# Optimization experiments

Measured on AMD Instinct MI355X. Metric: run time of the kernel, lower is better.

The kernel has to match this reference:

```python
import jax, jax.numpy as jnp
import numpy as np

N_NODES = 50000
N_EDGES = 800000
D_FEAT = 64
K_HOPS = 8


def setup_inputs() -> dict:
    key = jax.random.key(0)
    k1, k2 = jax.random.split(key)
    feature = jax.random.normal(k1, (N_NODES, D_FEAT), dtype=jnp.float32)
    edge_index = jax.random.randint(k2, (2, N_EDGES), 0, N_NODES, dtype=jnp.int32)
    return {"feature": feature, "edge_index": edge_index}


def reference(feature, edge_index):
    # with A_hat = D^{-1/2} (A + I) D^{-1/2} (add_remaining_self_loops + sym_norm).
    n = feature.shape[0]
    src, dst = edge_index[0], edge_index[1]
    # add_remaining_self_loops: drop any existing self-loop edges (weight -> 0)
    # and append a self loop of weight fill_value=1 for every node. Zeroing the
    # weight is mathematically identical to removing the edge.
    ew = jnp.where(src == dst, 0.0, 1.0).astype(feature.dtype)
    loop = jnp.arange(n, dtype=src.dtype)
    row = jnp.concatenate([src, loop])          # message source (x_j)
    col = jnp.concatenate([dst, loop])          # aggregation target (i)
    w = jnp.concatenate([ew, jnp.ones((n,), dtype=feature.dtype)])
    # symmetric normalization: deg over row, norm = d^-1/2[row] * w * d^-1/2[col]
    deg = jax.ops.segment_sum(w, row, num_segments=n)
    deg_inv_sqrt = jnp.where(deg > 0, jax.lax.rsqrt(deg), 0.0)
    norm = deg_inv_sqrt[row] * w * deg_inv_sqrt[col]  # [E+N]

    xs = [feature]
    x = feature
    for _ in range(K_HOPS):  # small fixed K, structural loop
        # gather-scale-scatter_add: out[i] = sum_{(j,i) in E} norm * x[j]
        x = jax.ops.segment_sum(norm[:, None] * x[row], col, num_segments=n)
        xs.append(x)
    return jnp.concatenate(xs, axis=1)  # [N, (K+1)*D]
```

## Files before the change

kernel.cpp:

```cpp
#include <hip/hip_runtime.h>
#include <hip/hip_fp16.h>

#define N_NODES 50000
#define N_EDGES 800000
#define D_FEAT 64
#define K_HOPS 8
#define OUT_STRIDE ((K_HOPS + 1) * D_FEAT)
#define NPART 128
#define CHUNK (N_EDGES / NPART)
#define NWORD (N_NODES / 2)

#define SCAN_WORDS 512
#define SCAN_NB ((NWORD + SCAN_WORDS - 1) / SCAN_WORDS)

#define ALIGN256(x) (((x) + 255) & ~(size_t)255)
static const size_t OFF_PSRC  = 0;
static const size_t OFF_PDST  = OFF_PSRC  + (size_t)NPART * NWORD * 4;
static const size_t OFF_BASES = OFF_PDST  + (size_t)NPART * NWORD * 4;
static const size_t OFF_OFF   = ALIGN256(OFF_BASES + (size_t)NPART * N_NODES * 4);
static const size_t OFF_BSUM  = ALIGN256(OFF_OFF   + (size_t)(N_NODES + 1) * 4);
static const size_t OFF_TOTW  = ALIGN256(OFF_BSUM  + 64 * 4);
static const size_t OFF_DINV  = ALIGN256(OFF_TOTW  + (size_t)NWORD * 4);
static const size_t OFF_CSR   = ALIGN256(OFF_DINV  + (size_t)N_NODES * 4);
static const size_t OFF_XA    = ALIGN256(OFF_CSR   + (size_t)N_EDGES * 4);
static const size_t OFF_XB    = ALIGN256(OFF_XA + (size_t)(N_NODES + 1) * D_FEAT * 2);

__device__ __forceinline__ unsigned pack_h2(float a, float b) {
    union { __half2 h; unsigned u; } c;
    c.h = __floats2half2_rn(a, b);
    return c.u;
}
__device__ __forceinline__ float2 unpack_h2(unsigned u) {
    union { unsigned u; __half2 h; } c;
    c.u = u;
    return __half22float2(c.h);
}


__global__ __launch_bounds__(256, 1) void k_hist(const int* __restrict__ src,
                                                 const int* __restrict__ dst,
                                                 unsigned* __restrict__ psrc,
                                                 unsigned* __restrict__ pdst) {
    __shared__ unsigned h[NWORD];
    int t = threadIdx.x;
    int base = blockIdx.x * CHUNK;
    for (int w = t; w < NWORD; w += 256) h[w] = 0u;
    __syncthreads();
    for (int j = t; j < CHUNK; j += 256) {
        int s = src[base + j], d = dst[base + j];
        if (s != d) atomicAdd(&h[s >> 1], (s & 1) ? 65536u : 1u);
    }
    __syncthreads();
    unsigned* o1 = psrc + (size_t)blockIdx.x * NWORD;
    for (int w = t; w < NWORD; w += 256) o1[w] = h[w];
    __syncthreads();
    for (int w = t; w < NWORD; w += 256) h[w] = 0u;
    __syncthreads();
    for (int j = t; j < CHUNK; j += 256) {
        int s = src[base + j], d = dst[base + j];
        if (s != d) atomicAdd(&h[d >> 1], (d & 1) ? 65536u : 1u);
    }
    __syncthreads();
    unsigned* o2 = pdst + (size_t)blockIdx.x * NWORD;
    for (int w = t; w < NWORD; w += 256) o2[w] = h[w];
}

__global__ void k_deg(const unsigned* __restrict__ psrc, float* __restrict__ dinv) {
    int w = blockIdx.x * blockDim.x + threadIdx.x;
    if (w >= NWORD) return;
    unsigned s0 = 0, s1 = 0, s2 = 0, s3 = 0;
    #pragma unroll 4
    for (int c = 0; c < NPART; c += 4) {
        s0 += psrc[(size_t)(c + 0) * NWORD + w];
        s1 += psrc[(size_t)(c + 1) * NWORD + w];
        s2 += psrc[(size_t)(c + 2) * NWORD + w];
        s3 += psrc[(size_t)(c + 3) * NWORD + w];
    }
    unsigned s = (s0 + s1) + (s2 + s3);
    dinv[2 * w + 0] = rsqrtf((float)((s & 0xffffu) + 1u));
    dinv[2 * w + 1] = rsqrtf((float)((s >> 16) + 1u));
}

__global__ void k_tot(const unsigned* __restrict__ pdst, unsigned* __restrict__ totW) {
    int w = blockIdx.x * blockDim.x + threadIdx.x;
    if (w >= NWORD) return;
    unsigned s0 = 0, s1 = 0, s2 = 0, s3 = 0;
    #pragma unroll 4
    for (int c = 0; c < NPART; c += 4) {
        s0 += pdst[(size_t)(c + 0) * NWORD + w];
        s1 += pdst[(size_t)(c + 1) * NWORD + w];
        s2 += pdst[(size_t)(c + 2) * NWORD + w];
        s3 += pdst[(size_t)(c + 3) * NWORD + w];
    }
    totW[w] = (s0 + s1) + (s2 + s3);
}

__global__ void k_scan_sums(const unsigned* __restrict__ totW, int* __restrict__ bsum) {
    __shared__ int lds[256];
    int b = blockIdx.x, t = threadIdx.x;
    int wend = min((b + 1) * SCAN_WORDS, NWORD);
    int tot = 0;
    for (int w = b * SCAN_WORDS + t; w < wend; w += 256) {
        unsigned v = totW[w];
        tot += (int)(v & 0xffffu) + (int)(v >> 16);
    }
    lds[t] = tot; __syncthreads();
    for (int str = 128; str > 0; str >>= 1) {
        if (t < str) lds[t] += lds[t + str];
        __syncthreads();
    }
    if (t == 0) bsum[b] = lds[0];
}

__global__ void k_scan_top(int* __restrict__ bsum) {
    int lane = threadIdx.x;
    int orig = (lane < SCAN_NB) ? bsum[lane] : 0;
    int v = orig;
    for (int d = 1; d < 64; d <<= 1) {
        int u = __shfl_up(v, d, 64);
        if (lane >= d) v += u;
    }
    if (lane < SCAN_NB) bsum[lane] = v - orig;
}

__global__ void k_scan_downA(const unsigned* __restrict__ totW, const int* __restrict__ bsum,
                             int* __restrict__ off) {
    __shared__ int lds[256];
    int b = blockIdx.x, t = threadIdx.x;
    int w0 = b * SCAN_WORDS + 2 * t;
    unsigned t0 = (w0 < NWORD) ? totW[w0] : 0u;
    unsigned t1 = (w0 + 1 < NWORD) ? totW[w0 + 1] : 0u;
    int n[4] = { (int)(t0 & 0xffffu), (int)(t0 >> 16),
                 (int)(t1 & 0xffffu), (int)(t1 >> 16) };
    int tsum = (n[0] + n[1]) + (n[2] + n[3]);
    lds[t] = tsum; __syncthreads();
    int x = tsum;
    for (int d = 1; d < 256; d <<= 1) {
        int u = (t >= d) ? lds[t - d] : 0;
        __syncthreads();
        x += u;
        lds[t] = x;
        __syncthreads();
    }
    int p = (x - tsum) + bsum[b];
    #pragma unroll
    for (int j = 0; j < 4; ++j) {
        int node = 2 * w0 + j;
        if (node < N_NODES) {
            off[node] = p;
            p += n[j];
        } else if (node == N_NODES) {
            off[node] = p;
        }
    }
}

__global__ void k_bases(const unsigned* __restrict__ pdst, const int* __restrict__ off,
                        int* __restrict__ bases) {
    int node = blockIdx.x * blockDim.x + threadIdx.x;
    if (node >= N_NODES) return;
    int w = node >> 1;
    bool hi = node & 1;
    int acc = off[node];
    for (int c = 0; c < NPART; ++c) {
        bases[(size_t)c * N_NODES + node] = acc;
        unsigned v = pdst[(size_t)c * NWORD + w];
        acc += hi ? (int)(v >> 16) : (int)(v & 0xffffu);
    }
}

__global__ __launch_bounds__(256, 1) void k_scatter(const int* __restrict__ src,
                                                    const int* __restrict__ dst,
                                                    const int* __restrict__ bases,
                                                    int* __restrict__ csr) {
    __shared__ unsigned h[NWORD];
    int t = threadIdx.x;
    int base = blockIdx.x * CHUNK;
    const int* bp = bases + (size_t)blockIdx.x * N_NODES;
    for (int w = t; w < NWORD; w += 256) h[w] = 0u;
    __syncthreads();
    for (int j = t; j < CHUNK; j += 256) {
        int s = src[base + j], d = dst[base + j];
        if (s == d) continue;
        unsigned old = atomicAdd(&h[d >> 1], (d & 1) ? 65536u : 1u);
        unsigned pw = (d & 1) ? (old >> 16) : (old & 0xffffu);
        csr[bp[d] + (int)pw] = s;
    }
}


__global__ void k_x0(const float4* __restrict__ feat4, float4* __restrict__ out4,
                     uint2* __restrict__ y0, const float* __restrict__ dinv) {
    int t = blockIdx.x * blockDim.x + threadIdx.x;
    if (t >= (N_NODES + 1) * 16) return;
    int row = t >> 4;
    if (row < N_NODES) {
        float4 v = feat4[t];
        out4[(size_t)row * (OUT_STRIDE / 4) + (t & 15)] = v;
        float di = dinv[row];
        uint2 w;
        w.x = pack_h2(v.x * di, v.y * di);
        w.y = pack_h2(v.z * di, v.w * di);
        y0[t] = w;
    } else {
        y0[t] = make_uint2(0u, 0u);
    }
}

template <bool WRITE_HALF>
__global__ __launch_bounds__(256) void k_hop4(
    const uint2* __restrict__ yin,
    float4* __restrict__ outcol4,
    uint2* __restrict__ yout,
    const int* __restrict__ off, const int* __restrict__ csr,
    const float* __restrict__ dinv) {
    int qw = (blockIdx.x * blockDim.x + threadIdx.x) >> 6;
    int lane = threadIdx.x & 63;
    int f = lane & 15;
    int node = qw * 4 + (lane >> 4);
    int e0 = off[node], e1 = off[node + 1];
    float di = dinv[node];
    uint2 sv = yin[node * 16 + f];
    float2 lo = unpack_h2(sv.x), hi = unpack_h2(sv.y);
    float a0 = lo.x, a1 = lo.y, a2 = hi.x, a3 = hi.y;

    int nm = e1 - e0;
    #pragma unroll
    for (int d = 32; d; d >>= 1) nm = max(nm, __shfl_xor(nm, d, 64));

    auto FETCH = [&](int j) -> int {
        int idx = e0 + j;
        int c = csr[idx < e1 ? idx : 0];
        return (idx < e1) ? c : N_NODES;
    };

    int c0 = FETCH(0), c1 = FETCH(1), c2 = FETCH(2), c3 = FETCH(3);
    for (int j = 0; j < nm; j += 4) {
        int d0 = FETCH(j + 4), d1 = FETCH(j + 5), d2 = FETCH(j + 6), d3 = FETCH(j + 7);
        uint2 q0 = yin[c0 * 16 + f];
        uint2 q1 = yin[c1 * 16 + f];
        uint2 q2 = yin[c2 * 16 + f];
        uint2 q3 = yin[c3 * 16 + f];
        float2 t;
        t = unpack_h2(q0.x); a0 += t.x; a1 += t.y;
        t = unpack_h2(q0.y); a2 += t.x; a3 += t.y;
        t = unpack_h2(q1.x); a0 += t.x; a1 += t.y;
        t = unpack_h2(q1.y); a2 += t.x; a3 += t.y;
        t = unpack_h2(q2.x); a0 += t.x; a1 += t.y;
        t = unpack_h2(q2.y); a2 += t.x; a3 += t.y;
        t = unpack_h2(q3.x); a0 += t.x; a1 += t.y;
        t = unpack_h2(q3.y); a2 += t.x; a3 += t.y;
        c0 = d0; c1 = d1; c2 = d2; c3 = d3;
    }

    outcol4[(size_t)node * (OUT_STRIDE / 4) + f] =
        make_float4(di * a0, di * a1, di * a2, di * a3);
    if (WRITE_HALF) {
        float di2 = di * di;
        uint2 w;
        w.x = pack_h2(di2 * a0, di2 * a1);
        w.y = pack_h2(di2 * a2, di2 * a3);
        yout[node * 16 + f] = w;
        if (blockIdx.x == 0 && threadIdx.x < 16)
            yout[N_NODES * 16 + threadIdx.x] = make_uint2(0u, 0u);
    }
}


extern "C" void kernel_launch(void* const* d_in, const int* in_sizes, int n_in,
                              void* d_out, int out_size, void* d_ws, size_t ws_size,
                              hipStream_t stream) {
    const float* feature = (const float*)d_in[0];
    const int* edge = (const int*)d_in[1];
    const int* src = edge;
    const int* dst = edge + N_EDGES;
    float* out = (float*)d_out;
    char* ws = (char*)d_ws;

    unsigned* psrc  = (unsigned*)(ws + OFF_PSRC);
    unsigned* pdst  = (unsigned*)(ws + OFF_PDST);
    int*      bases = (int*)(ws + OFF_BASES);
    int*      off   = (int*)(ws + OFF_OFF);
    int*      bsum  = (int*)(ws + OFF_BSUM);
    unsigned* totW  = (unsigned*)(ws + OFF_TOTW);
    float*    dinv  = (float*)(ws + OFF_DINV);
    int*      csr   = (int*)(ws + OFF_CSR);
    uint2*    xa    = (uint2*)(ws + OFF_XA);
    uint2*    xb    = (uint2*)(ws + OFF_XB);

    const int TB = 256;
    k_hist<<<NPART, 256, 0, stream>>>(src, dst, psrc, pdst);
    k_deg<<<(NWORD + TB - 1) / TB, TB, 0, stream>>>(psrc, dinv);
    k_x0<<<((N_NODES + 1) * 16 + TB - 1) / TB, TB, 0, stream>>>(
        (const float4*)feature, (float4*)out, xb, dinv);
    k_tot<<<(NWORD + TB - 1) / TB, TB, 0, stream>>>(pdst, totW);
    k_scan_sums<<<SCAN_NB, 256, 0, stream>>>(totW, bsum);
    k_scan_top<<<1, 64, 0, stream>>>(bsum);
    k_scan_downA<<<SCAN_NB, 256, 0, stream>>>(totW, bsum, off);
    k_bases<<<(N_NODES + TB - 1) / TB, TB, 0, stream>>>(pdst, off, bases);
    k_scatter<<<NPART, 256, 0, stream>>>(src, dst, bases, csr);
    const int hop_blocks = (N_NODES / 4) * 64 / TB;
    for (int k = 1; k <= K_HOPS; ++k) {
        const uint2* yin = (k & 1) ? xb : xa;
        uint2* yout      = (k & 1) ? xa : xb;
        float4* outcol4 = (float4*)out + (size_t)k * 16;
        if (k < K_HOPS)
            k_hop4<true><<<hop_blocks, TB, 0, stream>>>(yin, outcol4, yout, off, csr, dinv);
        else
            k_hop4<false><<<hop_blocks, TB, 0, stream>>>(yin, outcol4, nullptr, off, csr, dinv);
    }
}
```

Before: 354.8 us.

## Sort nodes by degree for hop load balance and merge src/dst histograms

Packs src and dst degree counts into one 8-bit-per-field histogram pass, removing a second edge scan and a reduction kernel. Adds a counting sort of nodes by in-degree (bucketed with node&3) and has the hop kernel process nodes through this permutation, so the four nodes sharing a wavefront have similar edge counts and less loop divergence. Costs a few small setup kernels and less contiguous per-wave memory access. The 8-bit counters assume per-partition degree stays below 256.

```diff
diff --git a/kernel.cpp b/kernel.cpp
--- a/kernel.cpp
+++ b/kernel.cpp
@@ -14,14 +14,16 @@
 #define SCAN_NB ((NWORD + SCAN_WORDS - 1) / SCAN_WORDS)
 
 #define ALIGN256(x) (((x) + 255) & ~(size_t)255)
-static const size_t OFF_PSRC  = 0;
-static const size_t OFF_PDST  = OFF_PSRC  + (size_t)NPART * NWORD * 4;
-static const size_t OFF_BASES = OFF_PDST  + (size_t)NPART * NWORD * 4;
+static const size_t OFF_P     = 0;
+static const size_t OFF_BASES = OFF_P + (size_t)NPART * NWORD * 4;
 static const size_t OFF_OFF   = ALIGN256(OFF_BASES + (size_t)NPART * N_NODES * 4);
 static const size_t OFF_BSUM  = ALIGN256(OFF_OFF   + (size_t)(N_NODES + 1) * 4);
 static const size_t OFF_TOTW  = ALIGN256(OFF_BSUM  + 64 * 4);
 static const size_t OFF_DINV  = ALIGN256(OFF_TOTW  + (size_t)NWORD * 4);
-static const size_t OFF_CSR   = ALIGN256(OFF_DINV  + (size_t)N_NODES * 4);
+static const size_t OFF_DCNT  = ALIGN256(OFF_DINV  + (size_t)N_NODES * 4);
+static const size_t OFF_DWORK = ALIGN256(OFF_DCNT  + 256 * 4);
+static const size_t OFF_PERM  = ALIGN256(OFF_DWORK + 256 * 4);
+static const size_t OFF_CSR   = ALIGN256(OFF_PERM  + (size_t)N_NODES * 4);
 static const size_t OFF_XA    = ALIGN256(OFF_CSR   + (size_t)N_EDGES * 4);
 static const size_t OFF_XB    = ALIGN256(OFF_XA + (size_t)(N_NODES + 1) * D_FEAT * 2);
 
@@ -39,8 +41,7 @@
 
 __global__ __launch_bounds__(256, 1) void k_hist(const int* __restrict__ src,
                                                  const int* __restrict__ dst,
-                                                 unsigned* __restrict__ psrc,
-                                                 unsigned* __restrict__ pdst) {
+                                                 unsigned* __restrict__ p) {
     __shared__ unsigned h[NWORD];
     int t = threadIdx.x;
     int base = blockIdx.x * CHUNK;
@@ -48,51 +49,32 @@
     __syncthreads();
     for (int j = t; j < CHUNK; j += 256) {
         int s = src[base + j], d = dst[base + j];
-        if (s != d) atomicAdd(&h[s >> 1], (s & 1) ? 65536u : 1u);
+        if (s != d) {
+            atomicAdd(&h[s >> 1], 1u << (8 * (s & 1)));
+            atomicAdd(&h[d >> 1], 65536u << (8 * (d & 1)));
+        }
     }
     __syncthreads();
-    unsigned* o1 = psrc + (size_t)blockIdx.x * NWORD;
-    for (int w = t; w < NWORD; w += 256) o1[w] = h[w];
-    __syncthreads();
-    for (int w = t; w < NWORD; w += 256) h[w] = 0u;
-    __syncthreads();
-    for (int j = t; j < CHUNK; j += 256) {
-        int s = src[base + j], d = dst[base + j];
-        if (s != d) atomicAdd(&h[d >> 1], (d & 1) ? 65536u : 1u);
-    }
-    __syncthreads();
-    unsigned* o2 = pdst + (size_t)blockIdx.x * NWORD;
-    for (int w = t; w < NWORD; w += 256) o2[w] = h[w];
-}
-
-__global__ void k_deg(const unsigned* __restrict__ psrc, float* __restrict__ dinv) {
+    unsigned* o = p + (size_t)blockIdx.x * NWORD;
+    for (int w = t; w < NWORD; w += 256) o[w] = h[w];
+}
+
+__global__ void k_sum(const unsigned* __restrict__ p, float* __restrict__ dinv,
+                      unsigned* __restrict__ totW) {
     int w = blockIdx.x * blockDim.x + threadIdx.x;
     if (w >= NWORD) return;
     unsigned s0 = 0, s1 = 0, s2 = 0, s3 = 0;
     #pragma unroll 4
     for (int c = 0; c < NPART; c += 4) {
-        s0 += psrc[(size_t)(c + 0) * NWORD + w];
-        s1 += psrc[(size_t)(c + 1) * NWORD + w];
-        s2 += psrc[(size_t)(c + 2) * NWORD + w];
-        s3 += psrc[(size_t)(c + 3) * NWORD + w];
+        s0 += p[(size_t)(c + 0) * NWORD + w];
+        s1 += p[(size_t)(c + 1) * NWORD + w];
+        s2 += p[(size_t)(c + 2) * NWORD + w];
+        s3 += p[(size_t)(c + 3) * NWORD + w];
     }
     unsigned s = (s0 + s1) + (s2 + s3);
-    dinv[2 * w + 0] = rsqrtf((float)((s & 0xffffu) + 1u));
-    dinv[2 * w + 1] = rsqrtf((float)((s >> 16) + 1u));
-}
-
-__global__ void k_tot(const unsigned* __restrict__ pdst, unsigned* __restrict__ totW) {
-    int w = blockIdx.x * blockDim.x + threadIdx.x;
-    if (w >= NWORD) return;
-    unsigned s0 = 0, s1 = 0, s2 = 0, s3 = 0;
-    #pragma unroll 4
-    for (int c = 0; c < NPART; c += 4) {
-        s0 += pdst[(size_t)(c + 0) * NWORD + w];
-        s1 += pdst[(size_t)(c + 1) * NWORD + w];
-        s2 += pdst[(size_t)(c + 2) * NWORD + w];
-        s3 += pdst[(size_t)(c + 3) * NWORD + w];
-    }
-    totW[w] = (s0 + s1) + (s2 + s3);
+    dinv[2 * w + 0] = rsqrtf((float)((s & 0xffu) + 1u));
+    dinv[2 * w + 1] = rsqrtf((float)(((s >> 8) & 0xffu) + 1u));
+    totW[w] = ((s >> 16) & 0xffu) | ((s >> 24) << 16);
 }
 
 __global__ void k_scan_sums(const unsigned* __restrict__ totW, int* __restrict__ bsum) {
@@ -142,30 +124,29 @@
         lds[t] = x;
         __syncthreads();
     }
-    int p = (x - tsum) + bsum[b];
+    int pfx = (x - tsum) + bsum[b];
     #pragma unroll
     for (int j = 0; j < 4; ++j) {
         int node = 2 * w0 + j;
         if (node < N_NODES) {
-            off[node] = p;
-            p += n[j];
+            off[node] = pfx;
+            pfx += n[j];
         } else if (node == N_NODES) {
-            off[node] = p;
+            off[node] = pfx;
         }
     }
 }
 
-__global__ void k_bases(const unsigned* __restrict__ pdst, const int* __restrict__ off,
+__global__ void k_bases(const unsigned* __restrict__ p, const int* __restrict__ off,
                         int* __restrict__ bases) {
     int node = blockIdx.x * blockDim.x + threadIdx.x;
     if (node >= N_NODES) return;
     int w = node >> 1;
-    bool hi = node & 1;
+    int sh = 16 + 8 * (node & 1);
     int acc = off[node];
     for (int c = 0; c < NPART; ++c) {
         bases[(size_t)c * N_NODES + node] = acc;
-        unsigned v = pdst[(size_t)c * NWORD + w];
-        acc += hi ? (int)(v >> 16) : (int)(v & 0xffffu);
+        acc += (int)((p[(size_t)c * NWORD + w] >> sh) & 0xffu);
     }
 }
 
@@ -188,6 +169,38 @@
     }
 }
 
+__global__ void k_dcount(const int* __restrict__ off, int* __restrict__ dcnt) {
+    int node = blockIdx.x * blockDim.x + threadIdx.x;
+    if (node >= N_NODES) return;
+    int deg = off[node + 1] - off[node];
+    atomicAdd(&dcnt[(min(deg, 63) << 2) | (node & 3)], 1);
+}
+
+__global__ void k_dscan(const int* __restrict__ dcnt, int* __restrict__ dwork) {
+    __shared__ int lds[256];
+    int t = threadIdx.x;
+    int v = dcnt[t];
+    lds[t] = v; __syncthreads();
+    int x = v;
+    for (int d = 1; d < 256; d <<= 1) {
+        int u = (t >= d) ? lds[t - d] : 0;
+        __syncthreads();
+        x += u;
+        lds[t] = x;
+        __syncthreads();
+    }
+    dwork[t] = x - v;
+}
+
+__global__ void k_dperm(const int* __restrict__ off, int* __restrict__ dwork,
+                        int* __restrict__ perm) {
+    int node = blockIdx.x * blockDim.x + threadIdx.x;
+    if (node >= N_NODES) return;
+    int deg = off[node + 1] - off[node];
+    int pos = atomicAdd(&dwork[(min(deg, 63) << 2) | (node & 3)], 1);
+    perm[pos] = node;
+}
+
 
 __global__ void k_x0(const float4* __restrict__ feat4, float4* __restrict__ out4,
                      uint2* __restrict__ y0, const float* __restrict__ dinv) {
@@ -213,11 +226,11 @@
     float4* __restrict__ outcol4,
     uint2* __restrict__ yout,
     const int* __restrict__ off, const int* __restrict__ csr,
-    const float* __restrict__ dinv) {
+    const float* __restrict__ dinv, const int* __restrict__ perm) {
     int qw = (blockIdx.x * blockDim.x + threadIdx.x) >> 6;
     int lane = threadIdx.x & 63;
     int f = lane & 15;
-    int node = qw * 4 + (lane >> 4);
+    int node = perm[qw * 4 + (lane >> 4)];
     int e0 = off[node], e1 = off[node + 1];
     float di = dinv[node];
     uint2 sv = yin[node * 16 + f];
@@ -277,36 +290,42 @@
     float* out = (float*)d_out;
     char* ws = (char*)d_ws;
 
-    unsigned* psrc  = (unsigned*)(ws + OFF_PSRC);
-    unsigned* pdst  = (unsigned*)(ws + OFF_PDST);
+    unsigned* p     = (unsigned*)(ws + OFF_P);
     int*      bases = (int*)(ws + OFF_BASES);
     int*      off   = (int*)(ws + OFF_OFF);
     int*      bsum  = (int*)(ws + OFF_BSUM);
     unsigned* totW  = (unsigned*)(ws + OFF_TOTW);
     float*    dinv  = (float*)(ws + OFF_DINV);
+    int*      dcnt  = (int*)(ws + OFF_DCNT);
+    int*      dwork = (int*)(ws + OFF_DWORK);
+    int*      perm  = (int*)(ws + OFF_PERM);
     int*      csr   = (int*)(ws + OFF_CSR);
     uint2*    xa    = (uint2*)(ws + OFF_XA);
     uint2*    xb    = (uint2*)(ws + OFF_XB);
 
     const int TB = 256;
-    k_hist<<<NPART, 256, 0, stream>>>(src, dst, psrc, pdst);
-    k_deg<<<(NWORD + TB - 1) / TB, TB, 0, stream>>>(psrc, dinv);
+    const int NB_NODES = (N_NODES + TB - 1) / TB;
+    hipMemsetAsync(dcnt, 0, 256 * 4, stream);
+    k_hist<<<NPART, 256, 0, stream>>>(src, dst, p);
+    k_sum<<<(NWORD + TB - 1) / TB, TB, 0, stream>>>(p, dinv, totW);
     k_x0<<<((N_NODES + 1) * 16 + TB - 1) / TB, TB, 0, stream>>>(
         (const float4*)feature, (float4*)out, xb, dinv);
-    k_tot<<<(NWORD + TB - 1) / TB, TB, 0, stream>>>(pdst, totW);
     k_scan_sums<<<SCAN_NB, 256, 0, stream>>>(totW, bsum);
     k_scan_top<<<1, 64, 0, stream>>>(bsum);
     k_scan_downA<<<SCAN_NB, 256, 0, stream>>>(totW, bsum, off);
-    k_bases<<<(N_NODES + TB - 1) / TB, TB, 0, stream>>>(pdst, off, bases);
+    k_bases<<<NB_NODES, TB, 0, stream>>>(p, off, bases);
     k_scatter<<<NPART, 256, 0, stream>>>(src, dst, bases, csr);
+    k_dcount<<<NB_NODES, TB, 0, stream>>>(off, dcnt);
+    k_dscan<<<1, 256, 0, stream>>>(dcnt, dwork);
+    k_dperm<<<NB_NODES, TB, 0, stream>>>(off, dwork, perm);
     const int hop_blocks = (N_NODES / 4) * 64 / TB;
     for (int k = 1; k <= K_HOPS; ++k) {
         const uint2* yin = (k & 1) ? xb : xa;
         uint2* yout      = (k & 1) ? xa : xb;
         float4* outcol4 = (float4*)out + (size_t)k * 16;
         if (k < K_HOPS)
-            k_hop4<true><<<hop_blocks, TB, 0, stream>>>(yin, outcol4, yout, off, csr, dinv);
+            k_hop4<true><<<hop_blocks, TB, 0, stream>>>(yin, outcol4, yout, off, csr, dinv, perm);
         else
-            k_hop4<false><<<hop_blocks, TB, 0, stream>>>(yin, outcol4, nullptr, off, csr, dinv);
-    }
-}
+            k_hop4<false><<<hop_blocks, TB, 0, stream>>>(yin, outcol4, nullptr, off, csr, dinv, perm);
+    }
+}
```

After: 440.9 us. 24.3% more time.
